# Kernel tuning notes

Hardware: AMD Instinct MI355X
Metric: run time of the kernel (lower is better)

Reference implementation:

```python
import jax, jax.numpy as jnp
import numpy as np

N, D_IN, D, K = 8192, 1024, 256, 30
SCALE = D ** (-0.5)


def setup_inputs() -> dict:
    key = jax.random.key(0)
    ks = jax.random.split(key, 10)
    p = lambda k, sh: (jax.random.normal(k, sh, dtype=jnp.float32) * 0.02)
    return {
        'x_path': jax.random.normal(ks[0], (N, D_IN), dtype=jnp.float32),
        'W_fc1': p(ks[1], (D_IN, D)), 'b_fc1': jnp.zeros((D,), jnp.float32),
        'W_fc2': p(ks[2], (D, D)),   'b_fc2': jnp.zeros((D,), jnp.float32),
        'W_head': p(ks[3], (D, D)),  'b_head': jnp.zeros((D,), jnp.float32),
        'W_tail': p(ks[4], (D, D)),  'b_tail': jnp.zeros((D,), jnp.float32),
        'W_lin1': p(ks[5], (D, D)),  'b_lin1': jnp.zeros((D,), jnp.float32),
        'W_lin2': p(ks[6], (D, D)),  'b_lin2': jnp.zeros((D,), jnp.float32),
        'W_att1': p(ks[7], (D, D // 2)), 'b_att1': jnp.zeros((D // 2,), jnp.float32),
        'W_att2': p(ks[8], (D // 2, 1)), 'b_att2': jnp.zeros((1,), jnp.float32),
    }


def reference(x_path, W_fc1, b_fc1, W_fc2, b_fc2, W_head, b_head, W_tail, b_tail,
              W_lin1, b_lin1, W_lin2, b_lin2, W_att1, b_att1, W_att2, b_att2):
    # pathology_fc (eval mode, dropout = identity): 1024 -> 256 -> 256
    h = jax.nn.relu(x_path @ W_fc1 + b_fc1)
    h = jax.nn.relu(h @ W_fc2 + b_fc2)                      # [N, D]

    e_h = h @ W_head + b_head                               # [N, D]
    e_t = h @ W_tail + b_tail                               # [N, D]

    # pairwise scores + topk neighbor selection
    attn_logit = (e_h * SCALE) @ e_t.T                      # [N, N]
    topk_w, topk_i = jax.lax.top_k(attn_logit, K)           # [N, K]
    topk_prob = jax.nn.softmax(topk_w, axis=-1)             # [N, K]

    Nb_h = e_t[topk_i]                                      # gather neighbors [N, K, D]

    # gated message construction
    eh_r = topk_prob[..., None] * Nb_h + (1.0 - topk_prob)[..., None] * e_h[:, None, :]
    gate = jnp.tanh(e_h[:, None, :] + eh_r)                 # [N, K, D]

    # torch.einsum('ijkl,ijkm->ijk', Nb_h, gate): l and m summed independently
    ka_weight = Nb_h.sum(-1) * gate.sum(-1)                 # [N, K]
    ka_prob = jax.nn.softmax(ka_weight, axis=-1)            # [N, K]
    e_Nh = jnp.einsum('nk,nkd->nd', ka_prob, Nb_h)          # [N, D]

    sum_emb = jax.nn.relu((e_h + e_Nh) @ W_lin1 + b_lin1)
    bi_emb = jax.nn.relu((e_h * e_Nh) @ W_lin2 + b_lin2)
    e = sum_emb + bi_emb                                    # [N, D]

    # GlobalAttention readout
    att = jax.nn.leaky_relu(e @ W_att1 + b_att1, 0.01) @ W_att2 + b_att2   # [N, 1]
    a = jax.nn.softmax(att, axis=0)                         # softmax over nodes
    e_g = (a * e).sum(0)                                    # [D]
    return e, e_g
```

## Files before the change

kernel.cpp:

```cpp
#include <hip/hip_runtime.h>
#include <math.h>

#define NN   8192
#define DIN  1024
#define DD   256
#define TOPK 30
#define KP   40
#define CAP  88
#define NINF -3e38f

typedef short s8v  __attribute__((ext_vector_type(8)));
typedef float f16v __attribute__((ext_vector_type(16)));

__device__ __forceinline__ float wred_sum(float v) {
  v += __shfl_down(v, 32); v += __shfl_down(v, 16); v += __shfl_down(v, 8);
  v += __shfl_down(v, 4);  v += __shfl_down(v, 2);  v += __shfl_down(v, 1);
  return v;
}
__device__ __forceinline__ float wred_max(float v) {
  v = fmaxf(v, __shfl_down(v, 32)); v = fmaxf(v, __shfl_down(v, 16));
  v = fmaxf(v, __shfl_down(v, 8));  v = fmaxf(v, __shfl_down(v, 4));
  v = fmaxf(v, __shfl_down(v, 2));  v = fmaxf(v, __shfl_down(v, 1));
  return v;
}
__device__ __forceinline__ float tanh_fast(float x) {
  return 1.f - 2.f / (__expf(2.f * x) + 1.f);
}
__device__ __forceinline__ unsigned short f2bf(float x) {
  union { float f; unsigned int u; } v; v.f = x;
  unsigned int r = v.u + 0x7FFF + ((v.u >> 16) & 1);
  return (unsigned short)(r >> 16);
}
__device__ __forceinline__ bool pair_gt(float v, int i, float pv, int pi) {
  return (v > pv) || (v == pv && i < pi);
}
__device__ __forceinline__ unsigned key_pack(float f, int col) {
  unsigned b = __float_as_uint(f);
  unsigned u = ((int)b < 0) ? ~b : (b | 0x80000000u);
  return (u & 0xFFFFE000u) | (unsigned)col;
}

template<int ACT>
__global__ __launch_bounds__(128, 4)
void gemm_k(const float* __restrict__ A,
            const float* __restrict__ B, const float* __restrict__ bias,
            float* __restrict__ C, int K, int NB)
{
  __shared__ float sA[32 * 36];
  __shared__ float sB[32 * 68];
  const int t  = threadIdx.x;
  const int rb = blockIdx.x * 32;
  const int cb = blockIdx.y * 64;
  const int tr = t >> 4;
  const int tc = t & 15;

  float acc[4][4];
#pragma unroll
  for (int u = 0; u < 4; ++u)
#pragma unroll
    for (int j = 0; j < 4; ++j) acc[u][j] = 0.f;

  const int sr  = t >> 2;
  const int sk2 = (t & 3) * 4;

  for (int kt = 0; kt < K; kt += 32) {
    __syncthreads();
    {
      const float* Ap = A + (size_t)(rb + sr) * K + kt;
      float4 va = *(const float4*)(Ap + sk2);
      float4 vb = *(const float4*)(Ap + sk2 + 16);
      sA[(sk2 + 0) * 36 + sr] = va.x; sA[(sk2 + 1) * 36 + sr] = va.y;
      sA[(sk2 + 2) * 36 + sr] = va.z; sA[(sk2 + 3) * 36 + sr] = va.w;
      sA[(sk2 + 16) * 36 + sr] = vb.x; sA[(sk2 + 17) * 36 + sr] = vb.y;
      sA[(sk2 + 18) * 36 + sr] = vb.z; sA[(sk2 + 19) * 36 + sr] = vb.w;
    }
    {
#pragma unroll
      for (int i = 0; i < 4; ++i) {
        const int f4 = t + 128 * i;
        const int k  = f4 >> 4;
        const int c4 = (f4 & 15) << 2;
        *(float4*)&sB[k * 68 + c4] = *(const float4*)&B[(size_t)(kt + k) * NB + cb + c4];
      }
    }
    __syncthreads();
#pragma unroll 8
    for (int k = 0; k < 32; ++k) {
      const float4 bv = *(const float4*)&sB[k * 68 + 4 * tc];
      const float4 av = *(const float4*)&sA[k * 36 + 4 * tr];
      const float a[4] = {av.x, av.y, av.z, av.w};
      const float b[4] = {bv.x, bv.y, bv.z, bv.w};
#pragma unroll
      for (int u = 0; u < 4; ++u)
#pragma unroll
        for (int j = 0; j < 4; ++j) acc[u][j] = fmaf(a[u], b[j], acc[u][j]);
    }
  }

  const float4 bz = *(const float4*)&bias[cb + 4 * tc];
  const float bb[4] = {bz.x, bz.y, bz.z, bz.w};
#pragma unroll
  for (int u = 0; u < 4; ++u) {
    const int row = rb + 4 * tr + u;
    float o[4];
#pragma unroll
    for (int j = 0; j < 4; ++j) {
      o[j] = acc[u][j] + bb[j];
      if (ACT) o[j] = fmaxf(o[j], 0.f);
    }
    float4 ov; ov.x = o[0]; ov.y = o[1]; ov.z = o[2]; ov.w = o[3];
    *(float4*)&C[(size_t)row * NB + cb + 4 * tc] = ov;
  }
}

__global__ __launch_bounds__(128, 4)
void gemm2_k(const float* __restrict__ A,
             const float* __restrict__ B1, const float* __restrict__ bias1,
             float* __restrict__ C1,
             const float* __restrict__ B2, const float* __restrict__ bias2,
             float* __restrict__ C2, int K, int NB)
{
  __shared__ float sA[32 * 36];
  __shared__ float sB1[32 * 68];
  __shared__ float sB2[32 * 68];
  const int t  = threadIdx.x;
  const int rb = blockIdx.x * 32;
  const int cb = blockIdx.y * 64;
  const int tr = t >> 4;
  const int tc = t & 15;

  float acc1[4][4], acc2[4][4];
#pragma unroll
  for (int u = 0; u < 4; ++u)
#pragma unroll
    for (int j = 0; j < 4; ++j) { acc1[u][j] = 0.f; acc2[u][j] = 0.f; }

  const int sr  = t >> 2;
  const int sk2 = (t & 3) * 4;

  for (int kt = 0; kt < K; kt += 32) {
    __syncthreads();
    {
      const float* Ap = A + (size_t)(rb + sr) * K + kt;
      float4 va = *(const float4*)(Ap + sk2);
      float4 vb = *(const float4*)(Ap + sk2 + 16);
      sA[(sk2 + 0) * 36 + sr] = va.x; sA[(sk2 + 1) * 36 + sr] = va.y;
      sA[(sk2 + 2) * 36 + sr] = va.z; sA[(sk2 + 3) * 36 + sr] = va.w;
      sA[(sk2 + 16) * 36 + sr] = vb.x; sA[(sk2 + 17) * 36 + sr] = vb.y;
      sA[(sk2 + 18) * 36 + sr] = vb.z; sA[(sk2 + 19) * 36 + sr] = vb.w;
    }
    {
#pragma unroll
      for (int i = 0; i < 4; ++i) {
        const int f4 = t + 128 * i;
        const int k  = f4 >> 4;
        const int c4 = (f4 & 15) << 2;
        *(float4*)&sB1[k * 68 + c4] = *(const float4*)&B1[(size_t)(kt + k) * NB + cb + c4];
        *(float4*)&sB2[k * 68 + c4] = *(const float4*)&B2[(size_t)(kt + k) * NB + cb + c4];
      }
    }
    __syncthreads();
#pragma unroll 4
    for (int k = 0; k < 32; ++k) {
      const float4 b1 = *(const float4*)&sB1[k * 68 + 4 * tc];
      const float4 b2 = *(const float4*)&sB2[k * 68 + 4 * tc];
      const float4 av = *(const float4*)&sA[k * 36 + 4 * tr];
      const float a[4] = {av.x, av.y, av.z, av.w};
      const float v1[4] = {b1.x, b1.y, b1.z, b1.w};
      const float v2[4] = {b2.x, b2.y, b2.z, b2.w};
#pragma unroll
      for (int u = 0; u < 4; ++u)
#pragma unroll
        for (int j = 0; j < 4; ++j) {
          acc1[u][j] = fmaf(a[u], v1[j], acc1[u][j]);
          acc2[u][j] = fmaf(a[u], v2[j], acc2[u][j]);
        }
    }
  }

  const float4 z1 = *(const float4*)&bias1[cb + 4 * tc];
  const float4 z2 = *(const float4*)&bias2[cb + 4 * tc];
  const float c1b[4] = {z1.x, z1.y, z1.z, z1.w};
  const float c2b[4] = {z2.x, z2.y, z2.z, z2.w};
#pragma unroll
  for (int u = 0; u < 4; ++u) {
    const int row = rb + 4 * tr + u;
    float4 o1, o2;
    o1.x = acc1[u][0] + c1b[0]; o1.y = acc1[u][1] + c1b[1];
    o1.z = acc1[u][2] + c1b[2]; o1.w = acc1[u][3] + c1b[3];
    o2.x = acc2[u][0] + c2b[0]; o2.y = acc2[u][1] + c2b[1];
    o2.z = acc2[u][2] + c2b[2]; o2.w = acc2[u][3] + c2b[3];
    *(float4*)&C1[(size_t)row * NB + cb + 4 * tc] = o1;
    *(float4*)&C2[(size_t)row * NB + cb + 4 * tc] = o2;
  }
}

__global__ __launch_bounds__(128, 4)
void gemm_lin_k(const float* __restrict__ Eh, const float* __restrict__ En,
                const float* __restrict__ B1, const float* __restrict__ bias1,
                const float* __restrict__ B2, const float* __restrict__ bias2,
                float* __restrict__ C, int K, int NB)
{
  __shared__ float sA1[32 * 36];
  __shared__ float sA2[32 * 36];
  __shared__ float sB1[32 * 68];
  __shared__ float sB2[32 * 68];
  const int t  = threadIdx.x;
  const int rb = blockIdx.x * 32;
  const int cb = blockIdx.y * 64;
  const int tr = t >> 4;
  const int tc = t & 15;

  float acc1[4][4], acc2[4][4];
#pragma unroll
  for (int u = 0; u < 4; ++u)
#pragma unroll
    for (int j = 0; j < 4; ++j) { acc1[u][j] = 0.f; acc2[u][j] = 0.f; }

  const int sr  = t >> 2;
  const int sk2 = (t & 3) * 4;

  for (int kt = 0; kt < K; kt += 32) {
    __syncthreads();
    {
      const float* Hp = Eh + (size_t)(rb + sr) * K + kt;
      const float* Np = En + (size_t)(rb + sr) * K + kt;
      const float4 ha = *(const float4*)(Hp + sk2);
      const float4 hb = *(const float4*)(Hp + sk2 + 16);
      const float4 na = *(const float4*)(Np + sk2);
      const float4 nb = *(const float4*)(Np + sk2 + 16);
      sA1[(sk2 + 0) * 36 + sr] = ha.x + na.x; sA2[(sk2 + 0) * 36 + sr] = ha.x * na.x;
      sA1[(sk2 + 1) * 36 + sr] = ha.y + na.y; sA2[(sk2 + 1) * 36 + sr] = ha.y * na.y;
      sA1[(sk2 + 2) * 36 + sr] = ha.z + na.z; sA2[(sk2 + 2) * 36 + sr] = ha.z * na.z;
      sA1[(sk2 + 3) * 36 + sr] = ha.w + na.w; sA2[(sk2 + 3) * 36 + sr] = ha.w * na.w;
      sA1[(sk2 + 16) * 36 + sr] = hb.x + nb.x; sA2[(sk2 + 16) * 36 + sr] = hb.x * nb.x;
      sA1[(sk2 + 17) * 36 + sr] = hb.y + nb.y; sA2[(sk2 + 17) * 36 + sr] = hb.y * nb.y;
      sA1[(sk2 + 18) * 36 + sr] = hb.z + nb.z; sA2[(sk2 + 18) * 36 + sr] = hb.z * nb.z;
      sA1[(sk2 + 19) * 36 + sr] = hb.w + nb.w; sA2[(sk2 + 19) * 36 + sr] = hb.w * nb.w;
    }
    {
#pragma unroll
      for (int i = 0; i < 4; ++i) {
        const int f4 = t + 128 * i;
        const int k  = f4 >> 4;
        const int c4 = (f4 & 15) << 2;
        *(float4*)&sB1[k * 68 + c4] = *(const float4*)&B1[(size_t)(kt + k) * NB + cb + c4];
        *(float4*)&sB2[k * 68 + c4] = *(const float4*)&B2[(size_t)(kt + k) * NB + cb + c4];
      }
    }
    __syncthreads();
#pragma unroll 4
    for (int k = 0; k < 32; ++k) {
      const float4 b1 = *(const float4*)&sB1[k * 68 + 4 * tc];
      const float4 b2 = *(const float4*)&sB2[k * 68 + 4 * tc];
      const float4 a1 = *(const float4*)&sA1[k * 36 + 4 * tr];
      const float4 a2 = *(const float4*)&sA2[k * 36 + 4 * tr];
      const float x1[4] = {a1.x, a1.y, a1.z, a1.w};
      const float x2[4] = {a2.x, a2.y, a2.z, a2.w};
      const float v1[4] = {b1.x, b1.y, b1.z, b1.w};
      const float v2[4] = {b2.x, b2.y, b2.z, b2.w};
#pragma unroll
      for (int u = 0; u < 4; ++u)
#pragma unroll
        for (int j = 0; j < 4; ++j) {
          acc1[u][j] = fmaf(x1[u], v1[j], acc1[u][j]);
          acc2[u][j] = fmaf(x2[u], v2[j], acc2[u][j]);
        }
    }
  }

  const float4 z1 = *(const float4*)&bias1[cb + 4 * tc];
  const float4 z2 = *(const float4*)&bias2[cb + 4 * tc];
  const float c1b[4] = {z1.x, z1.y, z1.z, z1.w};
  const float c2b[4] = {z2.x, z2.y, z2.z, z2.w};
#pragma unroll
  for (int u = 0; u < 4; ++u) {
    const int row = rb + 4 * tr + u;
    float4 ov;
    ov.x = fmaxf(acc1[u][0] + c1b[0], 0.f) + fmaxf(acc2[u][0] + c2b[0], 0.f);
    ov.y = fmaxf(acc1[u][1] + c1b[1], 0.f) + fmaxf(acc2[u][1] + c2b[1], 0.f);
    ov.z = fmaxf(acc1[u][2] + c1b[2], 0.f) + fmaxf(acc2[u][2] + c2b[2], 0.f);
    ov.w = fmaxf(acc1[u][3] + c1b[3], 0.f) + fmaxf(acc2[u][3] + c2b[3], 0.f);
    *(float4*)&C[(size_t)row * NB + cb + 4 * tc] = ov;
  }
}

__global__ __launch_bounds__(256)
void pack_frag_k(const float* __restrict__ srcA, unsigned short* __restrict__ dstA,
                 const float* __restrict__ srcB, unsigned short* __restrict__ dstB)
{
  const float* src = blockIdx.y ? srcB : srcA;
  unsigned short* dst = blockIdx.y ? dstB : dstA;
  const int c = blockIdx.x * 256 + threadIdx.x;
  const int l = c & 63;
  const int W = (c >> 6) & 15;
  const int T = c >> 10;
  const int col = T * 32 + (l & 31);
  const int k0  = W * 16 + ((l >> 5) << 3);
  const float4 a = *(const float4*)&src[(size_t)col * DD + k0];
  const float4 b = *(const float4*)&src[(size_t)col * DD + k0 + 4];
  uint4 o;
  o.x = (unsigned)f2bf(a.x) | ((unsigned)f2bf(a.y) << 16);
  o.y = (unsigned)f2bf(a.z) | ((unsigned)f2bf(a.w) << 16);
  o.z = (unsigned)f2bf(b.x) | ((unsigned)f2bf(b.y) << 16);
  o.w = (unsigned)f2bf(b.z) | ((unsigned)f2bf(b.w) << 16);
  *(uint4*)&dst[(size_t)c * 8] = o;
}

__global__ __launch_bounds__(256)
void rowsum_k(const float* __restrict__ et, float* __restrict__ rs)
{
  const int t = threadIdx.x, lane = t & 63, w = t >> 6;
  const int n = blockIdx.x * 4 + w;
  const float4 v = *(const float4*)&et[(size_t)n * DD + lane * 4];
  float s = v.x + v.y + v.z + v.w;
  s = wred_sum(s);
  if (lane == 0) rs[n] = s;
}

__global__ __launch_bounds__(512, 4)
void score_cand_k(const unsigned short* __restrict__ ehF,
                  const unsigned short* __restrict__ etF,
                  unsigned* __restrict__ gCand)
{
  __shared__ unsigned sBuf[32 * CAP];
  __shared__ unsigned sK[32][KP];
  __shared__ unsigned sThrK[32];
  __shared__ int      sCnt[32];

  const int t = threadIdx.x, lane = t & 63, w = t >> 6;
  const int g  = blockIdx.x;
  const int sy = blockIdx.y;
  const int tile0 = sy * 128;
  const s8v* eh8 = (const s8v*)ehF;
  const s8v* et8 = (const s8v*)etF;

  s8v af[16];
#pragma unroll
  for (int W = 0; W < 16; ++W)
    af[W] = eh8[((size_t)g * 16 + W) * 64 + lane];

  for (int idx = t; idx < 32 * KP; idx += 512) ((unsigned*)sK)[idx] = 0u;
  if (t < 32) { sThrK[t] = 0u; sCnt[t] = 0; }
  __syncthreads();

  const int rq = 4 * (lane >> 5);
  const int colLane = lane & 31;

  int tb = 0;
  for (int rnd = 0; rnd < 7; ++rnd) {
    const int ntile = (rnd == 0) ? 2 : (2 << (rnd - 1));
    for (int p = w; p < ntile; p += 8) {
      const int T = tile0 + tb + p;
      const s8v* bp = et8 + (size_t)T * 1024 + lane;
      f16v c;
#pragma unroll
      for (int i = 0; i < 16; ++i) c[i] = 0.f;
      {
        s8v b[8];
#pragma unroll
        for (int q = 0; q < 8; ++q) b[q] = bp[q * 64];
#pragma unroll
        for (int q = 0; q < 8; ++q)
          c = __builtin_amdgcn_mfma_f32_32x32x16_bf16(af[q], b[q], c, 0, 0, 0);
#pragma unroll
        for (int q = 0; q < 8; ++q) b[q] = bp[(8 + q) * 64];
#pragma unroll
        for (int q = 0; q < 8; ++q)
          c = __builtin_amdgcn_mfma_f32_32x32x16_bf16(af[8 + q], b[q], c, 0, 0, 0);
      }
      const int col = T * 32 + colLane;
#pragma unroll
      for (int r = 0; r < 16; ++r) {
        const int row = (r & 3) + 8 * (r >> 2) + rq;
        const unsigned key = key_pack(c[r], col);
        if (key > sThrK[row]) {
          const int ix = atomicAdd(&sCnt[row], 1);
          if (ix < CAP) sBuf[row * CAP + ix] = key;
        }
      }
    }
    __syncthreads();

#pragma unroll 1
    for (int rp = 0; rp < 2; ++rp) {
      const int ra = 4 * w + 2 * rp;
      const int rc = ra + 1;
      const int cA = min(sCnt[ra], CAP);
      const int cB = min(sCnt[rc], CAP);
      unsigned a0 = (lane < KP) ? sK[ra][lane]
                                : ((lane - KP) < cA ? sBuf[ra * CAP + (lane - KP)] : 0u);
      unsigned a1 = ((24 + lane) < cA) ? sBuf[ra * CAP + 24 + lane] : 0u;
      unsigned b0 = (lane < KP) ? sK[rc][lane]
                                : ((lane - KP) < cB ? sBuf[rc * CAP + (lane - KP)] : 0u);
      unsigned b1 = ((24 + lane) < cB) ? sBuf[rc * CAP + 24 + lane] : 0u;
#pragma unroll
      for (int k = 2; k <= 128; k <<= 1) {
#pragma unroll
        for (int j = k >> 1; j >= 1; j >>= 1) {
          if (j == 64) {
            unsigned mx = max(a0, a1), mn = min(a0, a1); a0 = mx; a1 = mn;
            mx = max(b0, b1); mn = min(b0, b1); b0 = mx; b1 = mn;
          } else {
            const unsigned pa0 = (unsigned)__shfl_xor((int)a0, j);
            const unsigned pa1 = (unsigned)__shfl_xor((int)a1, j);
            const unsigned pb0 = (unsigned)__shfl_xor((int)b0, j);
            const unsigned pb1 = (unsigned)__shfl_xor((int)b1, j);
            const bool km0 = (((lane & k) == 0)        == ((lane & j) == 0));
            const bool km1 = ((((64 + lane) & k) == 0) == ((lane & j) == 0));
            a0 = km0 ? max(a0, pa0) : min(a0, pa0);
            a1 = km1 ? max(a1, pa1) : min(a1, pa1);
            b0 = km0 ? max(b0, pb0) : min(b0, pb0);
            b1 = km1 ? max(b1, pb1) : min(b1, pb1);
          }
        }
      }
      if (rnd < 6) {
        if (lane < KP) { sK[ra][lane] = a0; sK[rc][lane] = b0; }
        if (lane == KP - 1) { sThrK[ra] = a0; sThrK[rc] = b0; }
        if (lane == 0) { sCnt[ra] = 0; sCnt[rc] = 0; }
      } else {
        if (lane < KP) {
          gCand[(((size_t)g * 2 + sy) * 32 + ra) * KP + lane] = a0;
          gCand[(((size_t)g * 2 + sy) * 32 + rc) * KP + lane] = b0;
        }
      }
    }
    __syncthreads();
    tb += ntile;
  }
}

__global__ __launch_bounds__(512, 2)
void cand_merge_k(const unsigned* __restrict__ gCand,
                  const float* __restrict__ e_h, const float* __restrict__ e_t,
                  float* __restrict__ topv_g, int* __restrict__ topi_g)
{
  __shared__ float    sEh[16 * 256];
  __shared__ unsigned sK40[16][KP];
  __shared__ float    sRes[16][KP];
  const int t = threadIdx.x, lane = t & 63, w = t >> 6;
  const int g = blockIdx.x, rb = g * 32;
  const int r0 = blockIdx.y * 16;

  for (int i = t; i < 1024; i += 512)
    ((float4*)sEh)[i] = ((const float4*)(e_h + (size_t)(rb + r0) * 256))[i];

#pragma unroll 1
  for (int rp = 0; rp < 2; ++rp) {
    const int lr = 2 * w + rp;
    const int r  = r0 + lr;
    unsigned v0, v1;
    {
      const int m = lane;
      const int s = m / 40, q = m - s * 40;
      v0 = gCand[(((size_t)g * 2 + s) * 32 + r) * KP + q];
    }
    {
      const int m = 64 + lane;
      if (m < 80) {
        const int q = m - 40;
        v1 = gCand[(((size_t)g * 2 + 1) * 32 + r) * KP + q];
      } else v1 = 0u;
    }
#pragma unroll
    for (int k = 2; k <= 128; k <<= 1) {
#pragma unroll
      for (int j = k >> 1; j >= 1; j >>= 1) {
        if (j == 64) {
          const unsigned mx = max(v0, v1), mn = min(v0, v1);
          v0 = mx; v1 = mn;
        } else {
          const unsigned p0 = (unsigned)__shfl_xor((int)v0, j);
          const unsigned p1 = (unsigned)__shfl_xor((int)v1, j);
          const bool km0 = (((lane & k) == 0)        == ((lane & j) == 0));
          const bool km1 = ((((64 + lane) & k) == 0) == ((lane & j) == 0));
          v0 = km0 ? max(v0, p0) : min(v0, p0);
          v1 = km1 ? max(v1, p1) : min(v1, p1);
        }
      }
    }
    if (lane < KP) sK40[lr][lane] = v0;
  }
  __syncthreads();

  for (int i = t; i < 16 * KP; i += 512) {
    const int lr = i / KP, q = i - lr * KP;
    const int c = (int)(sK40[lr][q] & 0x1FFFu);
    const float* et = &e_t[(size_t)c * 256];
    const float* eh = &sEh[lr * 256];
    float acc = 0.f;
#pragma unroll 8
    for (int d = 0; d < 64; ++d) {
      const float4 a = *(const float4*)&eh[d * 4];
      const float4 b = *(const float4*)&et[d * 4];
      acc = fmaf(a.x, b.x, acc); acc = fmaf(a.y, b.y, acc);
      acc = fmaf(a.z, b.z, acc); acc = fmaf(a.w, b.w, acc);
    }
    sRes[lr][q] = acc * 0.0625f;
  }
  __syncthreads();

#pragma unroll 1
  for (int rp = 0; rp < 2; ++rp) {
    const int lr = 2 * w + rp;
    float v; int c;
    if (lane < KP) { v = sRes[lr][lane]; c = (int)(sK40[lr][lane] & 0x1FFFu); }
    else           { v = NINF;           c = 0x40000000 + lane; }
#pragma unroll
    for (int k = 2; k <= 64; k <<= 1) {
#pragma unroll
      for (int j = k >> 1; j >= 1; j >>= 1) {
        const float pv = __shfl_xor(v, j);
        const int   pc = __shfl_xor(c, j);
        const bool km = (((lane & k) == 0) == ((lane & j) == 0));
        const bool gt = pair_gt(v, c, pv, pc);
        const bool keep = (km == gt);
        v = keep ? v : pv; c = keep ? c : pc;
      }
    }
    if (lane < TOPK) {
      topv_g[(size_t)(rb + r0 + lr) * TOPK + lane] = v;
      topi_g[(size_t)(rb + r0 + lr) * TOPK + lane] = c;
    }
  }
}

__global__ __launch_bounds__(256)
void message_k(const float* __restrict__ e_h, const float* __restrict__ e_t,
               const float* __restrict__ rs, const float* __restrict__ tv_g,
               const int* __restrict__ ti_g, float* __restrict__ e_Nh)
{
  __shared__ float sP[TOPK];
  __shared__ int   sI[TOPK];
  __shared__ float sW[TOPK];
  __shared__ float wpart[TOPK][4];
  const int n = blockIdx.x;
  const int t = threadIdx.x, lane = t & 63, w = t >> 6;

  if (w == 0) {
    const float v = (lane < TOPK) ? tv_g[(size_t)n * TOPK + lane] : NINF;
    float m = wred_max(v); m = __shfl(m, 0);
    const float p = (lane < TOPK) ? __expf(v - m) : 0.f;
    float s = wred_sum(p); s = __shfl(s, 0);
    if (lane < TOPK) { sP[lane] = p / s; sI[lane] = ti_g[(size_t)n * TOPK + lane]; }
  }
  __syncthreads();

  const float eh = e_h[(size_t)n * DD + t];
  float nbv[TOPK];
  float gg[TOPK];
#pragma unroll
  for (int k = 0; k < TOPK; ++k) {
    const int   j = sI[k];
    const float p = sP[k];
    const float nb = e_t[(size_t)j * DD + t];
    nbv[k] = nb;
    gg[k] = tanh_fast((2.f - p) * eh + p * nb);
  }
#pragma unroll
  for (int off = 32; off >= 1; off >>= 1)
#pragma unroll
    for (int k = 0; k < TOPK; ++k)
      gg[k] += __shfl_down(gg[k], off);
  if (lane == 0)
#pragma unroll
    for (int k = 0; k < TOPK; ++k) wpart[k][w] = gg[k];
  __syncthreads();

  if (w == 0) {
    float kw = NINF;
    if (lane < TOPK) {
      const float gs = wpart[lane][0] + wpart[lane][1] + wpart[lane][2] + wpart[lane][3];
      kw = rs[sI[lane]] * gs;
    }
    float m = wred_max(kw); m = __shfl(m, 0);
    const float p = (lane < TOPK) ? __expf(kw - m) : 0.f;
    float s = wred_sum(p); s = __shfl(s, 0);
    if (lane < TOPK) sW[lane] = p / s;
  }
  __syncthreads();

  float o = 0.f;
#pragma unroll
  for (int k = 0; k < TOPK; ++k) o = fmaf(sW[k], nbv[k], o);
  e_Nh[(size_t)n * DD + t] = o;
}

__global__ __launch_bounds__(256)
void att_k(const float* __restrict__ e, const float* __restrict__ W1,
           const float* __restrict__ b1, const float* __restrict__ W2,
           const float* __restrict__ b2, float* __restrict__ att)
{
  const int t = threadIdx.x;
  const int q = t >> 7;
  const int m = t & 127;
  const int lane = t & 63, w = t >> 6;
  const int n0 = blockIdx.x * 8 + q * 4;
  float acc[4] = {0.f, 0.f, 0.f, 0.f};
  for (int d = 0; d < DD; ++d) {
    const float wv = W1[d * 128 + m];
#pragma unroll
    for (int rr = 0; rr < 4; ++rr)
      acc[rr] = fmaf(e[(size_t)(n0 + rr) * DD + d], wv, acc[rr]);
  }
  const float b1m = b1[m], w2m = W2[m];
  __shared__ float part[4][4];
#pragma unroll
  for (int rr = 0; rr < 4; ++rr) {
    float v = acc[rr] + b1m;
    v = (v > 0.f) ? v : 0.01f * v;
    v *= w2m;
    v = wred_sum(v);
    if (lane == 0) part[w][rr] = v;
  }
  __syncthreads();
  if (t < 8) {
    const int qq = t >> 2, rr = t & 3;
    att[blockIdx.x * 8 + qq * 4 + rr] = part[qq * 2][rr] + part[qq * 2 + 1][rr] + b2[0];
  }
}

__global__ __launch_bounds__(1024)
void smax_prep_k(const float* __restrict__ att, float* __restrict__ stats,
                 float* __restrict__ eg)
{
  __shared__ float red[16];
  __shared__ float mg;
  const int t = threadIdx.x, lane = t & 63, w = t >> 6;
  float m = NINF;
#pragma unroll
  for (int i = 0; i < 8; ++i) m = fmaxf(m, att[t + 1024 * i]);
  m = wred_max(m);
  if (lane == 0) red[w] = m;
  __syncthreads();
  if (t == 0) {
    float mm = red[0];
    for (int i = 1; i < 16; ++i) mm = fmaxf(mm, red[i]);
    mg = mm;
  }
  __syncthreads();
  const float mm = mg;
  float s = 0.f;
#pragma unroll
  for (int i = 0; i < 8; ++i) s += __expf(att[t + 1024 * i] - mm);
  s = wred_sum(s);
  __syncthreads();
  if (lane == 0) red[w] = s;
  __syncthreads();
  if (t == 0) {
    float ss = 0.f;
    for (int i = 0; i < 16; ++i) ss += red[i];
    stats[0] = mm; stats[1] = ss;
  }
  if (t < DD) eg[t] = 0.f;
}

__global__ __launch_bounds__(256)
void eg_k(const float* __restrict__ att, const float* __restrict__ stats,
          const float* __restrict__ e, float* __restrict__ eg)
{
  const int t = threadIdx.x;
  const float m = stats[0], inv = 1.f / stats[1];
  float acc = 0.f;
  const int n0 = blockIdx.x * 128;
  for (int r = 0; r < 128; ++r) {
    const int n = n0 + r;
    acc = fmaf(__expf(att[n] - m), e[(size_t)n * DD + t], acc);
  }
  atomicAdd(&eg[t], acc * inv);
}

extern "C" void kernel_launch(void* const* d_in, const int* in_sizes, int n_in,
                              void* d_out, int out_size, void* d_ws, size_t ws_size,
                              hipStream_t stream)
{
  const float* x      = (const float*)d_in[0];
  const float* W_fc1  = (const float*)d_in[1];
  const float* b_fc1  = (const float*)d_in[2];
  const float* W_fc2  = (const float*)d_in[3];
  const float* b_fc2  = (const float*)d_in[4];
  const float* W_head = (const float*)d_in[5];
  const float* b_head = (const float*)d_in[6];
  const float* W_tail = (const float*)d_in[7];
  const float* b_tail = (const float*)d_in[8];
  const float* W_lin1 = (const float*)d_in[9];
  const float* b_lin1 = (const float*)d_in[10];
  const float* W_lin2 = (const float*)d_in[11];
  const float* b_lin2 = (const float*)d_in[12];
  const float* W_att1 = (const float*)d_in[13];
  const float* b_att1 = (const float*)d_in[14];
  const float* W_att2 = (const float*)d_in[15];
  const float* b_att2 = (const float*)d_in[16];

  float* out_e  = (float*)d_out;
  float* out_eg = out_e + (size_t)NN * DD;

  float* ws = (float*)d_ws;
  const size_t F = (size_t)NN * DD;
  float* e_h   = ws;
  float* e_t   = ws + F;
  float* e_Nh  = ws + 2 * F;
  float* bufA  = ws + 3 * F;
  float* bufB  = ws + 4 * F;
  float* rs    = ws + 5 * F;
  float* att   = rs + NN;
  float* stats = att + NN;
  float* topv  = stats + 16;
  int*   topi  = (int*)(topv + (size_t)NN * TOPK);

  unsigned short* ehF = (unsigned short*)bufA;
  unsigned short* etF = ehF + F;
  unsigned* gCand = (unsigned*)bufB;

  const dim3 blk(256);
  const dim3 gblk(128);
  const dim3 gemmGrid(NN / 32, DD / 64);

  gemm_k<1><<<gemmGrid, gblk, 0, stream>>>(x,    W_fc1, b_fc1, bufA, DIN, DD);
  gemm_k<1><<<gemmGrid, gblk, 0, stream>>>(bufA, W_fc2, b_fc2, bufB, DD,  DD);
  gemm2_k<<<gemmGrid, gblk, 0, stream>>>(bufB, W_head, b_head, e_h,
                                         W_tail, b_tail, e_t, DD, DD);

  pack_frag_k<<<dim3(NN * DD / 8 / 256, 2), blk, 0, stream>>>(e_h, ehF, e_t, etF);
  rowsum_k<<<dim3(NN / 4), blk, 0, stream>>>(e_t, rs);

  score_cand_k<<<dim3(NN / 32, 2), dim3(512), 0, stream>>>(ehF, etF, gCand);
  cand_merge_k<<<dim3(NN / 32, 2), dim3(512), 0, stream>>>(gCand, e_h, e_t, topv, topi);

  message_k<<<dim3(NN), blk, 0, stream>>>(e_h, e_t, rs, topv, topi, e_Nh);

  gemm_lin_k<<<gemmGrid, gblk, 0, stream>>>(e_h, e_Nh, W_lin1, b_lin1,
                                            W_lin2, b_lin2, out_e, DD, DD);

  att_k<<<dim3(NN / 8), blk, 0, stream>>>(out_e, W_att1, b_att1, W_att2, b_att2, att);
  smax_prep_k<<<dim3(1), dim3(1024), 0, stream>>>(att, stats, out_eg);
  eg_k<<<dim3(64), blk, 0, stream>>>(att, stats, out_e, out_eg);
}
```

Baseline: 626.0 us.

## Fuse bf16 fragment packing and row sums into head/tail GEMM epilogue

```diff
diff --git a/kernel.cpp b/kernel.cpp
--- a/kernel.cpp
+++ b/kernel.cpp
@@ -118,7 +118,9 @@
              const float* __restrict__ B1, const float* __restrict__ bias1,
              float* __restrict__ C1,
              const float* __restrict__ B2, const float* __restrict__ bias2,
-             float* __restrict__ C2, int K, int NB)
+             float* __restrict__ C2,
+             unsigned short* __restrict__ F1, unsigned short* __restrict__ F2,
+             float* __restrict__ rs, int K, int NB)
 {
   __shared__ float sA[32 * 36];
   __shared__ float sB1[32 * 68];
@@ -182,16 +184,42 @@
   const float4 z2 = *(const float4*)&bias2[cb + 4 * tc];
   const float c1b[4] = {z1.x, z1.y, z1.z, z1.w};
   const float c2b[4] = {z2.x, z2.y, z2.z, z2.w};
+  const int Wf   = 4 * blockIdx.y + (tc >> 2);
+  const int lHi  = ((tc >> 1) & 1) << 5;
+  const int eOff = (tc & 1) << 2;
+  float rsum[4];
 #pragma unroll
   for (int u = 0; u < 4; ++u) {
     const int row = rb + 4 * tr + u;
-    float4 o1, o2;
-    o1.x = acc1[u][0] + c1b[0]; o1.y = acc1[u][1] + c1b[1];
-    o1.z = acc1[u][2] + c1b[2]; o1.w = acc1[u][3] + c1b[3];
-    o2.x = acc2[u][0] + c2b[0]; o2.y = acc2[u][1] + c2b[1];
-    o2.z = acc2[u][2] + c2b[2]; o2.w = acc2[u][3] + c2b[3];
-    *(float4*)&C1[(size_t)row * NB + cb + 4 * tc] = o1;
-    *(float4*)&C2[(size_t)row * NB + cb + 4 * tc] = o2;
+    float o1[4], o2[4];
+#pragma unroll
+    for (int j = 0; j < 4; ++j) {
+      o1[j] = acc1[u][j] + c1b[j];
+      o2[j] = acc2[u][j] + c2b[j];
+    }
+    rsum[u] = (o2[0] + o2[1]) + (o2[2] + o2[3]);
+    float4 w1; w1.x = o1[0]; w1.y = o1[1]; w1.z = o1[2]; w1.w = o1[3];
+    float4 w2; w2.x = o2[0]; w2.y = o2[1]; w2.z = o2[2]; w2.w = o2[3];
+    *(float4*)&C1[(size_t)row * NB + cb + 4 * tc] = w1;
+    *(float4*)&C2[(size_t)row * NB + cb + 4 * tc] = w2;
+    const int chunk = (blockIdx.x * 16 + Wf) * 64 + ((row & 31) | lHi);
+    uint2 p1, p2;
+    p1.x = (unsigned)f2bf(o1[0]) | ((unsigned)f2bf(o1[1]) << 16);
+    p1.y = (unsigned)f2bf(o1[2]) | ((unsigned)f2bf(o1[3]) << 16);
+    p2.x = (unsigned)f2bf(o2[0]) | ((unsigned)f2bf(o2[1]) << 16);
+    p2.y = (unsigned)f2bf(o2[2]) | ((unsigned)f2bf(o2[3]) << 16);
+    *(uint2*)&F1[(size_t)chunk * 8 + eOff] = p1;
+    *(uint2*)&F2[(size_t)chunk * 8 + eOff] = p2;
+  }
+#pragma unroll
+  for (int off = 8; off >= 1; off >>= 1)
+#pragma unroll
+    for (int u = 0; u < 4; ++u)
+      rsum[u] += __shfl_down(rsum[u], off);
+  if (tc == 0) {
+#pragma unroll
+    for (int u = 0; u < 4; ++u)
+      atomicAdd(&rs[rb + 4 * tr + u], rsum[u]);
   }
 }
 
@@ -285,39 +313,6 @@
   }
 }
 
-__global__ __launch_bounds__(256)
-void pack_frag_k(const float* __restrict__ srcA, unsigned short* __restrict__ dstA,
-                 const float* __restrict__ srcB, unsigned short* __restrict__ dstB)
-{
-  const float* src = blockIdx.y ? srcB : srcA;
-  unsigned short* dst = blockIdx.y ? dstB : dstA;
-  const int c = blockIdx.x * 256 + threadIdx.x;
-  const int l = c & 63;
-  const int W = (c >> 6) & 15;
-  const int T = c >> 10;
-  const int col = T * 32 + (l & 31);
-  const int k0  = W * 16 + ((l >> 5) << 3);
-  const float4 a = *(const float4*)&src[(size_t)col * DD + k0];
-  const float4 b = *(const float4*)&src[(size_t)col * DD + k0 + 4];
-  uint4 o;
-  o.x = (unsigned)f2bf(a.x) | ((unsigned)f2bf(a.y) << 16);
-  o.y = (unsigned)f2bf(a.z) | ((unsigned)f2bf(a.w) << 16);
-  o.z = (unsigned)f2bf(b.x) | ((unsigned)f2bf(b.y) << 16);
-  o.w = (unsigned)f2bf(b.z) | ((unsigned)f2bf(b.w) << 16);
-  *(uint4*)&dst[(size_t)c * 8] = o;
-}
-
-__global__ __launch_bounds__(256)
-void rowsum_k(const float* __restrict__ et, float* __restrict__ rs)
-{
-  const int t = threadIdx.x, lane = t & 63, w = t >> 6;
-  const int n = blockIdx.x * 4 + w;
-  const float4 v = *(const float4*)&et[(size_t)n * DD + lane * 4];
-  float s = v.x + v.y + v.z + v.w;
-  s = wred_sum(s);
-  if (lane == 0) rs[n] = s;
-}
-
 __global__ __launch_bounds__(512, 4)
 void score_cand_k(const unsigned short* __restrict__ ehF,
                   const unsigned short* __restrict__ etF,
@@ -531,29 +526,24 @@
                const float* __restrict__ rs, const float* __restrict__ tv_g,
                const int* __restrict__ ti_g, float* __restrict__ e_Nh)
 {
-  __shared__ float sP[TOPK];
-  __shared__ int   sI[TOPK];
-  __shared__ float sW[TOPK];
   __shared__ float wpart[TOPK][4];
   const int n = blockIdx.x;
   const int t = threadIdx.x, lane = t & 63, w = t >> 6;
 
-  if (w == 0) {
-    const float v = (lane < TOPK) ? tv_g[(size_t)n * TOPK + lane] : NINF;
-    float m = wred_max(v); m = __shfl(m, 0);
-    const float p = (lane < TOPK) ? __expf(v - m) : 0.f;
-    float s = wred_sum(p); s = __shfl(s, 0);
-    if (lane < TOPK) { sP[lane] = p / s; sI[lane] = ti_g[(size_t)n * TOPK + lane]; }
-  }
-  __syncthreads();
+  const float v = (lane < TOPK) ? tv_g[(size_t)n * TOPK + lane] : NINF;
+  const int  ji = (lane < TOPK) ? ti_g[(size_t)n * TOPK + lane] : 0;
+  float m = wred_max(v); m = __shfl(m, 0);
+  float pe = (lane < TOPK) ? __expf(v - m) : 0.f;
+  float s = wred_sum(pe); s = __shfl(s, 0);
+  const float pk = pe / s;
 
   const float eh = e_h[(size_t)n * DD + t];
   float nbv[TOPK];
   float gg[TOPK];
 #pragma unroll
   for (int k = 0; k < TOPK; ++k) {
-    const int   j = sI[k];
-    const float p = sP[k];
+    const int   j = __shfl(ji, k);
+    const float p = __shfl(pk, k);
     const float nb = e_t[(size_t)j * DD + t];
     nbv[k] = nb;
     gg[k] = tanh_fast((2.f - p) * eh + p * nb);
@@ -568,22 +558,19 @@
     for (int k = 0; k < TOPK; ++k) wpart[k][w] = gg[k];
   __syncthreads();
 
-  if (w == 0) {
-    float kw = NINF;
-    if (lane < TOPK) {
-      const float gs = wpart[lane][0] + wpart[lane][1] + wpart[lane][2] + wpart[lane][3];
-      kw = rs[sI[lane]] * gs;
-    }
-    float m = wred_max(kw); m = __shfl(m, 0);
-    const float p = (lane < TOPK) ? __expf(kw - m) : 0.f;
-    float s = wred_sum(p); s = __shfl(s, 0);
-    if (lane < TOPK) sW[lane] = p / s;
-  }
-  __syncthreads();
+  float kw = NINF;
+  if (lane < TOPK) {
+    const float gs = wpart[lane][0] + wpart[lane][1] + wpart[lane][2] + wpart[lane][3];
+    kw = rs[ji] * gs;
+  }
+  float m2 = wred_max(kw); m2 = __shfl(m2, 0);
+  float p2 = (lane < TOPK) ? __expf(kw - m2) : 0.f;
+  float s2 = wred_sum(p2); s2 = __shfl(s2, 0);
+  const float wk = p2 / s2;
 
   float o = 0.f;
 #pragma unroll
-  for (int k = 0; k < TOPK; ++k) o = fmaf(sW[k], nbv[k], o);
+  for (int k = 0; k < TOPK; ++k) o = fmaf(__shfl(wk, k), nbv[k], o);
   e_Nh[(size_t)n * DD + t] = o;
 }
 
@@ -663,8 +650,8 @@
   const int t = threadIdx.x;
   const float m = stats[0], inv = 1.f / stats[1];
   float acc = 0.f;
-  const int n0 = blockIdx.x * 128;
-  for (int r = 0; r < 128; ++r) {
+  const int n0 = blockIdx.x * 32;
+  for (int r = 0; r < 32; ++r) {
     const int n = n0 + r;
     acc = fmaf(__expf(att[n] - m), e[(size_t)n * DD + t], acc);
   }
@@ -719,11 +706,11 @@
 
   gemm_k<1><<<gemmGrid, gblk, 0, stream>>>(x,    W_fc1, b_fc1, bufA, DIN, DD);
   gemm_k<1><<<gemmGrid, gblk, 0, stream>>>(bufA, W_fc2, b_fc2, bufB, DD,  DD);
+
+  hipMemsetAsync(rs, 0, NN * sizeof(float), stream);
+
   gemm2_k<<<gemmGrid, gblk, 0, stream>>>(bufB, W_head, b_head, e_h,
-                                         W_tail, b_tail, e_t, DD, DD);
-
-  pack_frag_k<<<dim3(NN * DD / 8 / 256, 2), blk, 0, stream>>>(e_h, ehF, e_t, etF);
-  rowsum_k<<<dim3(NN / 4), blk, 0, stream>>>(e_t, rs);
+                                         W_tail, b_tail, e_t, ehF, etF, rs, DD, DD);
 
   score_cand_k<<<dim3(NN / 32, 2), dim3(512), 0, stream>>>(ehF, etF, gCand);
   cand_merge_k<<<dim3(NN / 32, 2), dim3(512), 0, stream>>>(gCand, e_h, e_t, topv, topi);
@@ -735,5 +722,5 @@
 
   att_k<<<dim3(NN / 8), blk, 0, stream>>>(out_e, W_att1, b_att1, W_att2, b_att2, att);
   smax_prep_k<<<dim3(1), dim3(1024), 0, stream>>>(att, stats, out_eg);
-  eg_k<<<dim3(64), blk, 0, stream>>>(att, stats, out_e, out_eg);
-}
+  eg_k<<<dim3(NN / 32), blk, 0, stream>>>(att, stats, out_e, out_eg);
+}
```

Result: slower. 656.4 us (+4.9%).
